# Kernel optimization log

Measured on AMD Instinct MI355X. Metric: run time of the kernel, lower is better.

## Reference

```python
import jax, jax.numpy as jnp
import numpy as np
from jax import lax

B, C, H, W = 32, 256, 64, 64
EPS = 1e-5


def setup_inputs() -> dict:
    key = jax.random.key(0)
    ks = jax.random.split(key, 4)
    x = jax.random.normal(ks[0], (B, C, H, W), dtype=jnp.float32)
    def mk(k):
        kw, = jax.random.split(k, 1)
        w = jax.random.normal(kw, (1, 2, 7, 7), dtype=jnp.float32) * 0.1  # OIHW
        gamma = jnp.ones((1,), jnp.float32)
        beta = jnp.zeros((1,), jnp.float32)
        rmean = jnp.zeros((1,), jnp.float32)
        rvar = jnp.ones((1,), jnp.float32)
        return w, gamma, beta, rmean, rvar
    w1, g1, b1, m1, v1 = mk(ks[1])
    w2, g2, b2, m2, v2 = mk(ks[2])
    w3, g3, b3, m3, v3 = mk(ks[3])
    return dict(x=x,
                w1=w1, g1=g1, b1=b1, m1=m1, v1=v1,
                w2=w2, g2=g2, b2=b2, m2=m2, v2=v2,
                w3=w3, g3=g3, b3=b3, m3=m3, v3=v3)


def _conv_bn_sig(p, w, gamma, beta, mean, var):
    # p: [B,2,h,w]; 7x7 conv 2->1, pad 3, no bias; BN (inference); sigmoid
    y = lax.conv_general_dilated(p, w, window_strides=(1, 1),
                                 padding=[(3, 3), (3, 3)],
                                 dimension_numbers=('NCHW', 'OIHW', 'NCHW'))
    r = lambda t: t.reshape(1, -1, 1, 1)
    y = (y - r(mean)) * (r(gamma) / jnp.sqrt(r(var) + EPS)) + r(beta)
    return jax.nn.sigmoid(y)


def reference(x, w1, g1, b1, m1, v1, w2, g2, b2, m2, v2, w3, g3, b3, m3, v3):
    # In this implementation the permutes cancel: all three branches pool over C.
    mx = jnp.max(x, axis=1, keepdims=True)
    av = jnp.mean(x, axis=1, keepdims=True)
    pooled = jnp.concatenate([mx, av], axis=1)              # [B,2,H,W]
    a1 = _conv_bn_sig(pooled, w1, g1, b1, m1, v1)           # [B,1,H,W]
    p2 = jnp.transpose(pooled, (0, 1, 3, 2))                # [B,2,W,H]
    a2 = jnp.transpose(_conv_bn_sig(p2, w2, g2, b2, m2, v2), (0, 1, 3, 2))
    a3 = _conv_bn_sig(pooled, w3, g3, b3, m3, v3)
    att = (a1 + a2 + a3) / 3.0
    return x * att
```

## Files before the change

kernel.cpp:

```cpp
#include <hip/hip_runtime.h>
#include <math.h>

#define NB 32
#define NC 256
#define NH 64
#define NW 64
#define NHW (NH * NW)
#define EPS_ 1e-5f

typedef float f32x4 __attribute__((ext_vector_type(4)));

__global__ __launch_bounds__(512) void pool_k(const float* __restrict__ x,
                                              float* __restrict__ pooled) {
    const int tid = threadIdx.x;
    const int chunk = tid >> 6;
    const int lane = tid & 63;
    const int q = blockIdx.x * 64 + lane;
    const int b = q >> 10;
    const int hwq = q & 1023;

    const float4* __restrict__ xq = (const float4*)x;
    const int base = b * NC * (NHW / 4) + hwq;

    float4 mx = make_float4(-INFINITY, -INFINITY, -INFINITY, -INFINITY);
    float4 sm = make_float4(0.f, 0.f, 0.f, 0.f);
    const int c0 = chunk * 32;
    #pragma unroll 8
    for (int c = c0; c < c0 + 32; ++c) {
        float4 v = xq[base + c * (NHW / 4)];
        mx.x = fmaxf(mx.x, v.x); mx.y = fmaxf(mx.y, v.y);
        mx.z = fmaxf(mx.z, v.z); mx.w = fmaxf(mx.w, v.w);
        sm.x += v.x; sm.y += v.y; sm.z += v.z; sm.w += v.w;
    }

    __shared__ float4 smax[8][64];
    __shared__ float4 ssum[8][64];
    smax[chunk][lane] = mx;
    ssum[chunk][lane] = sm;
    __syncthreads();

    if (tid < 64) {
        float4 m = smax[0][tid];
        float4 s = ssum[0][tid];
        #pragma unroll
        for (int k = 1; k < 8; ++k) {
            float4 m2 = smax[k][tid];
            float4 s2 = ssum[k][tid];
            m.x = fmaxf(m.x, m2.x); m.y = fmaxf(m.y, m2.y);
            m.z = fmaxf(m.z, m2.z); m.w = fmaxf(m.w, m2.w);
            s.x += s2.x; s.y += s2.y; s.z += s2.z; s.w += s2.w;
        }
        const float inv = 1.f / (float)NC;
        float4 mean = make_float4(s.x * inv, s.y * inv, s.z * inv, s.w * inv);
        float4* __restrict__ pq = (float4*)pooled;
        pq[(b * 2 + 0) * (NHW / 4) + hwq] = m;
        pq[(b * 2 + 1) * (NHW / 4) + hwq] = mean;
    }
}

__global__ __launch_bounds__(256) void attmul_k(
    const float* __restrict__ x,
    const float* __restrict__ pooled,
    const float* __restrict__ w1, const float* __restrict__ g1,
    const float* __restrict__ be1, const float* __restrict__ m1,
    const float* __restrict__ v1,
    const float* __restrict__ w2, const float* __restrict__ g2,
    const float* __restrict__ be2, const float* __restrict__ m2,
    const float* __restrict__ v2,
    const float* __restrict__ w3, const float* __restrict__ g3,
    const float* __restrict__ be3, const float* __restrict__ m3,
    const float* __restrict__ v3,
    float* __restrict__ out) {
    const int b = blockIdx.x >> 6;
    const int h = blockIdx.x & 63;
    const int t = threadIdx.x;

    __shared__ float plds[7][2][72];
    __shared__ float att_s[64];

    #pragma unroll
    for (int k = 0; k < 4; ++k) {
        const int idx = t + k * 256;
        if (idx < 1008) {
            const int r = idx / 144;
            const int rem = idx - r * 144;
            const int ci = rem / 72;
            const int col = rem - ci * 72;
            const int y = h - 3 + r;
            const int xcol = col - 3;
            float v = 0.f;
            if ((unsigned)y < (unsigned)NH && (unsigned)xcol < (unsigned)NW)
                v = pooled[((b * 2 + ci) * NH + y) * NW + xcol];
            plds[r][ci][col] = v;
        }
    }
    __syncthreads();

    if (t < 64) {
        const int w = t;
        float s1 = 0.f, s2 = 0.f, s3 = 0.f;
        #pragma unroll
        for (int r = 0; r < 7; ++r) {
            #pragma unroll
            for (int ci = 0; ci < 2; ++ci) {
                #pragma unroll
                for (int dw = 0; dw < 7; ++dw) {
                    const float p = plds[r][ci][w + dw];
                    s1 = fmaf(p, w1[ci * 49 + r * 7 + dw], s1);
                    s2 = fmaf(p, w2[ci * 49 + dw * 7 + r], s2);
                    s3 = fmaf(p, w3[ci * 49 + r * 7 + dw], s3);
                }
            }
        }
        const float sc1 = g1[0] * rsqrtf(v1[0] + EPS_);
        const float sc2 = g2[0] * rsqrtf(v2[0] + EPS_);
        const float sc3 = g3[0] * rsqrtf(v3[0] + EPS_);
        const float y1 = (s1 - m1[0]) * sc1 + be1[0];
        const float y2 = (s2 - m2[0]) * sc2 + be2[0];
        const float y3 = (s3 - m3[0]) * sc3 + be3[0];
        const float a1 = 1.f / (1.f + expf(-y1));
        const float a2 = 1.f / (1.f + expf(-y2));
        const float a3 = 1.f / (1.f + expf(-y3));
        att_s[w] = (a1 + a2 + a3) * (1.f / 3.f);
    }
    __syncthreads();

    const f32x4* __restrict__ xq = (const f32x4*)x;
    f32x4* __restrict__ oq = (f32x4*)out;
    const f32x4* __restrict__ a4 = (const f32x4*)att_s;
    #pragma unroll 4
    for (int k = 0; k < 16; ++k) {
        const int j = t + k * 256;
        const int c = j >> 4;
        const int wq = j & 15;
        const int addr = (b * NC + c) * (NHW / 4) + h * 16 + wq;
        const f32x4 v = xq[addr];
        const f32x4 a = a4[wq];
        __builtin_nontemporal_store(v * a, &oq[addr]);
    }
}

extern "C" void kernel_launch(void* const* d_in, const int* in_sizes, int n_in,
                              void* d_out, int out_size, void* d_ws, size_t ws_size,
                              hipStream_t stream) {
    const float* x  = (const float*)d_in[0];
    const float* w1 = (const float*)d_in[1];
    const float* g1 = (const float*)d_in[2];
    const float* b1 = (const float*)d_in[3];
    const float* m1 = (const float*)d_in[4];
    const float* v1 = (const float*)d_in[5];
    const float* w2 = (const float*)d_in[6];
    const float* g2 = (const float*)d_in[7];
    const float* b2 = (const float*)d_in[8];
    const float* m2 = (const float*)d_in[9];
    const float* v2 = (const float*)d_in[10];
    const float* w3 = (const float*)d_in[11];
    const float* g3 = (const float*)d_in[12];
    const float* b3 = (const float*)d_in[13];
    const float* m3 = (const float*)d_in[14];
    const float* v3 = (const float*)d_in[15];
    float* out = (float*)d_out;

    float* pooled = (float*)d_ws;

    pool_k<<<NB * NHW / 4 / 64, 512, 0, stream>>>(x, pooled);
    attmul_k<<<NB * NH, 256, 0, stream>>>(x, pooled,
        w1, g1, b1, m1, v1, w2, g2, b2, m2, v2, w3, g3, b3, m3, v3, out);
}
```

Baseline: 286.0 us.

## Process four rows per block in attention-multiply kernel with full-wave conv

Each attmul block now covers four image rows instead of one, loading a 10-row pooled halo once and having all 256 threads compute the 7x7 convolutions (one row per wave). The multiply loop streams 1 KB contiguous rows per wave across channels, and each thread holds its attention vector in registers. This cuts redundant halo loads and leaves fewer threads idle during the conv. In exchange the grid shrinks to 512 blocks, which may reduce occupancy and latency hiding on a large GPU.

Measured after the change: 299.7 us. 4.8% more time.

```diff
diff --git a/kernel.cpp b/kernel.cpp
--- a/kernel.cpp
+++ b/kernel.cpp
@@ -71,44 +71,46 @@
     const float* __restrict__ be3, const float* __restrict__ m3,
     const float* __restrict__ v3,
     float* __restrict__ out) {
-    const int b = blockIdx.x >> 6;
-    const int h = blockIdx.x & 63;
+    const int b = blockIdx.x >> 4;
+    const int h4 = blockIdx.x & 15;
+    const int h0 = h4 * 4;
     const int t = threadIdx.x;
 
-    __shared__ float plds[7][2][72];
-    __shared__ float att_s[64];
+    __shared__ float plds[10][2][72];
+    __shared__ float att_s[256];
 
     #pragma unroll
-    for (int k = 0; k < 4; ++k) {
+    for (int k = 0; k < 6; ++k) {
         const int idx = t + k * 256;
-        if (idx < 1008) {
+        if (idx < 1440) {
             const int r = idx / 144;
             const int rem = idx - r * 144;
             const int ci = rem / 72;
             const int col = rem - ci * 72;
-            const int y = h - 3 + r;
-            const int xcol = col - 3;
+            const int y = h0 - 3 + r;
+            const int xc = col - 3;
             float v = 0.f;
-            if ((unsigned)y < (unsigned)NH && (unsigned)xcol < (unsigned)NW)
-                v = pooled[((b * 2 + ci) * NH + y) * NW + xcol];
+            if ((unsigned)y < (unsigned)NH && (unsigned)xc < (unsigned)NW)
+                v = pooled[((b * 2 + ci) * NH + y) * NW + xc];
             plds[r][ci][col] = v;
         }
     }
     __syncthreads();
 
-    if (t < 64) {
-        const int w = t;
+    {
+        const int r = t >> 6;
+        const int w = t & 63;
         float s1 = 0.f, s2 = 0.f, s3 = 0.f;
         #pragma unroll
-        for (int r = 0; r < 7; ++r) {
+        for (int dh = 0; dh < 7; ++dh) {
             #pragma unroll
             for (int ci = 0; ci < 2; ++ci) {
                 #pragma unroll
                 for (int dw = 0; dw < 7; ++dw) {
-                    const float p = plds[r][ci][w + dw];
-                    s1 = fmaf(p, w1[ci * 49 + r * 7 + dw], s1);
-                    s2 = fmaf(p, w2[ci * 49 + dw * 7 + r], s2);
-                    s3 = fmaf(p, w3[ci * 49 + r * 7 + dw], s3);
+                    const float p = plds[r + dh][ci][w + dw];
+                    s1 = fmaf(p, w1[ci * 49 + dh * 7 + dw], s1);
+                    s2 = fmaf(p, w2[ci * 49 + dw * 7 + dh], s2);
+                    s3 = fmaf(p, w3[ci * 49 + dh * 7 + dw], s3);
                 }
             }
         }
@@ -121,22 +123,22 @@
         const float a1 = 1.f / (1.f + expf(-y1));
         const float a2 = 1.f / (1.f + expf(-y2));
         const float a3 = 1.f / (1.f + expf(-y3));
-        att_s[w] = (a1 + a2 + a3) * (1.f / 3.f);
+        att_s[t] = (a1 + a2 + a3) * (1.f / 3.f);
     }
     __syncthreads();
 
     const f32x4* __restrict__ xq = (const f32x4*)x;
     f32x4* __restrict__ oq = (f32x4*)out;
     const f32x4* __restrict__ a4 = (const f32x4*)att_s;
-    #pragma unroll 4
-    for (int k = 0; k < 16; ++k) {
-        const int j = t + k * 256;
-        const int c = j >> 4;
-        const int wq = j & 15;
-        const int addr = (b * NC + c) * (NHW / 4) + h * 16 + wq;
+    const int wv = t >> 6;
+    const int l = t & 63;
+    const f32x4 a = a4[l];
+    int addr = (b * NC + wv) * (NHW / 4) + h4 * 64 + l;
+    #pragma unroll 8
+    for (int i = 0; i < 64; ++i) {
         const f32x4 v = xq[addr];
-        const f32x4 a = a4[wq];
         __builtin_nontemporal_store(v * a, &oq[addr]);
+        addr += 4 * (NHW / 4);
     }
 }
 
@@ -164,6 +166,6 @@
     float* pooled = (float*)d_ws;
 
     pool_k<<<NB * NHW / 4 / 64, 512, 0, stream>>>(x, pooled);
-    attmul_k<<<NB * NH, 256, 0, stream>>>(x, pooled,
+    attmul_k<<<NB * (NH / 4), 256, 0, stream>>>(x, pooled,
         w1, g1, b1, m1, v1, w2, g2, b2, m2, v2, w3, g3, b3, m3, v3, out);
 }
```
